# Kernel optimization log

Measured on AMD Instinct MI355X. Metric: run time of the kernel, lower is better.

## Reference

```python
import jax, jax.numpy as jnp
import numpy as np

N = 50000      # nodes
E = 400000     # edges
IN = 128       # in_channels
HID = 64       # hidden_channels (per head)
H = 4          # heads
OUT = 10       # classes
G = 64         # graphs in batch


def setup_inputs() -> dict:
    key = jax.random.key(0)
    ks = jax.random.split(key, 32)
    s = 0.05
    inp = {
        "x": jax.random.normal(ks[0], (N, IN), dtype=jnp.float32),
        "edge_index": jax.random.randint(ks[1], (2, E), 0, N, dtype=jnp.int32),
        "batch": jnp.sort(jax.random.randint(ks[2], (N,), 0, G, dtype=jnp.int32)),
    }
    # TransformerConv layer 1 params (in=IN -> heads*HID)
    d1 = H * HID
    inp["Wq1"] = jax.random.normal(ks[3], (IN, d1)) * s
    inp["bq1"] = jnp.zeros((d1,), jnp.float32)
    inp["Wk1"] = jax.random.normal(ks[4], (IN, d1)) * s
    inp["bk1"] = jnp.zeros((d1,), jnp.float32)
    inp["Wv1"] = jax.random.normal(ks[5], (IN, d1)) * s
    inp["bv1"] = jnp.zeros((d1,), jnp.float32)
    inp["Ws1"] = jax.random.normal(ks[6], (IN, d1)) * s   # root/skip weight
    inp["bs1"] = jnp.zeros((d1,), jnp.float32)
    # TransformerConv layer 2 params (in=H*HID -> heads*HID)
    inp["Wq2"] = jax.random.normal(ks[7], (d1, d1)) * s
    inp["bq2"] = jnp.zeros((d1,), jnp.float32)
    inp["Wk2"] = jax.random.normal(ks[8], (d1, d1)) * s
    inp["bk2"] = jnp.zeros((d1,), jnp.float32)
    inp["Wv2"] = jax.random.normal(ks[9], (d1, d1)) * s
    inp["bv2"] = jnp.zeros((d1,), jnp.float32)
    inp["Ws2"] = jax.random.normal(ks[10], (d1, d1)) * s
    inp["bs2"] = jnp.zeros((d1,), jnp.float32)
    # final classifier
    inp["Wl"] = jax.random.normal(ks[11], (d1, OUT)) * s
    inp["bl"] = jnp.zeros((OUT,), jnp.float32)
    return inp


def transformer_conv(x, src, dst, Wq, bq, Wk, bk, Wv, bv, Ws, bs):
    """PyG TransformerConv (concat=True, root_weight=True, beta=None, eval mode).
    src = edge_index[0] (source j), dst = edge_index[1] (target i).
    """
    n = x.shape[0]
    q = (x @ Wq + bq).reshape(n, H, HID)
    k = (x @ Wk + bk).reshape(n, H, HID)
    v = (x @ Wv + bv).reshape(n, H, HID)
    # per-edge attention logits [E, H]
    alpha = jnp.einsum('ehc,ehc->eh', q[dst], k[src]) / np.sqrt(HID).astype(np.float32)
    # scatter-softmax over incoming edges of each target node
    amax = jax.ops.segment_max(alpha, dst, num_segments=n)           # [N, H], -inf for isolated
    ex = jnp.exp(alpha - amax[dst])                                   # [E, H]
    denom = jax.ops.segment_sum(ex, dst, num_segments=n) + 1e-16      # [N, H]
    w = ex / denom[dst]                                               # normalized alpha [E, H]
    # scatter-sum aggregation of weighted values
    out = jax.ops.segment_sum(w[:, :, None] * v[src], dst, num_segments=n)  # [N, H, HID]
    out = out.reshape(n, H * HID)
    return out + (x @ Ws + bs)  # root/skip connection


def reference(x, edge_index, batch,
              Wq1, bq1, Wk1, bk1, Wv1, bv1, Ws1, bs1,
              Wq2, bq2, Wk2, bk2, Wv2, bv2, Ws2, bs2,
              Wl, bl):
    src, dst = edge_index[0], edge_index[1]
    h = jax.nn.elu(transformer_conv(x, src, dst, Wq1, bq1, Wk1, bk1, Wv1, bv1, Ws1, bs1))
    h = jax.nn.elu(transformer_conv(h, src, dst, Wq2, bq2, Wk2, bk2, Wv2, bv2, Ws2, bs2))
    # global mean pool per graph
    sums = jax.ops.segment_sum(h, batch, num_segments=G)              # [G, H*HID]
    cnt = jax.ops.segment_sum(jnp.ones((h.shape[0],), h.dtype), batch, num_segments=G)
    pooled = sums / jnp.maximum(cnt, 1.0)[:, None]
    logits = pooled @ Wl + bl
    return jax.nn.log_softmax(logits, axis=-1)
```

## Files before the change

kernel.cpp:

```cpp
#include <hip/hip_runtime.h>
#include <math.h>

constexpr int NN   = 50000;
constexpr int NE   = 400000;
constexpr int INC  = 128;
constexpr int NH   = 4;
constexpr int D1   = 256;
constexpr int D4   = 1024;
constexpr int NOUT = 10;
constexpr int NG   = 64;
constexpr int NB_SCAN = (NN + 255) / 256;


typedef __attribute__((ext_vector_type(8))) short bf16x8;
typedef __attribute__((ext_vector_type(4))) float f32x4;
typedef __attribute__((ext_vector_type(2))) float f32x2;

__device__ __forceinline__ short f2b(float f) {
  union { float f; unsigned int i; } v; v.f = f;
  unsigned int x = v.i;
  return (short)((x + 0x7FFFu + ((x >> 16) & 1u)) >> 16);
}
__device__ __forceinline__ float b2f(short u) {
  union { unsigned int i; float f; } v; v.i = ((unsigned int)(unsigned short)u) << 16;
  return v.f;
}
__device__ __forceinline__ float4 ld4b(const short* p) {
  short4 u = *(const short4*)p;
  return make_float4(b2f(u.x), b2f(u.y), b2f(u.z), b2f(u.w));
}
__device__ __forceinline__ int cvt_pk_bf16(float lo, float hi) {
  int r;
  asm volatile("v_cvt_pk_bf16_f32 %0, %1, %2" : "=v"(r) : "v"(lo), "v"(hi));
  return r;
}
__device__ __forceinline__ int pk_fp8x4(float a, float b, float c, float d) {
  int v = __builtin_amdgcn_cvt_pk_fp8_f32(a, b, 0, false);
  v = __builtin_amdgcn_cvt_pk_fp8_f32(c, d, v, true);
  return v;
}

__device__ __forceinline__ void gld_lds16(const short* g, short* l) {
  __builtin_amdgcn_global_load_lds(
      (const __attribute__((address_space(1))) unsigned int*)g,
      (__attribute__((address_space(3))) unsigned int*)l, 16, 0, 0);
}

constexpr int CVT_XB  = (NN * INC / 4 + 255) / 256;
constexpr int CVT_W1B = (4 * D1 * INC / 8 + 255) / 256;
constexpr int CVT_W2B = (4 * D1 * D1 / 8 + 255) / 256;
constexpr int CVT_BB  = 8;
constexpr int CVT_DB  = (NN + 255) / 256;
constexpr int CVT_FB  = 1;

__device__ __forceinline__ void wt_one8(const float* Wq, const float* Wk,
    const float* Wv, const float* Ws, short* Wt, int kbits, int i) {
  const int K = 1 << kbits;
  const int row = i >> (kbits - 3);
  const int k0 = (i & ((K >> 3) - 1)) << 3;
  int seg, n;
  if (row < 256)      { seg = 0; n = row; }
  else if (row < 768) { int j = row - 256, off = j & 7;
                        seg = (off >= 4) ? 2 : 1; n = (j >> 3) * 4 + (off & 3); }
  else                { seg = 3; n = row - 768; }
  const float* W = (seg == 0) ? Wq : (seg == 1) ? Wk : (seg == 2) ? Wv : Ws;
  short o[8];
#pragma unroll
  for (int kk = 0; kk < 8; kk++) o[kk] = f2b(W[(size_t)(k0 + kk) * D1 + n]);
  int4 pk;
  short* ps = (short*)&pk;
#pragma unroll
  for (int kk = 0; kk < 8; kk++) ps[kk] = o[kk];
  *(int4*)(Wt + (size_t)row * K + k0) = pk;
}

__global__ void cvt_all_k(const float* __restrict__ x, short* __restrict__ Xb,
    const float* __restrict__ Wq1, const float* __restrict__ Wk1,
    const float* __restrict__ Wv1, const float* __restrict__ Ws1,
    const float* __restrict__ Wq2, const float* __restrict__ Wk2,
    const float* __restrict__ Wv2, const float* __restrict__ Ws2,
    short* __restrict__ Wtc1, short* __restrict__ Wtc2,
    const float* __restrict__ bq1, const float* __restrict__ bk1,
    const float* __restrict__ bv1, const float* __restrict__ bs1,
    const float* __restrict__ bq2, const float* __restrict__ bk2,
    const float* __restrict__ bv2, const float* __restrict__ bs2,
    float* __restrict__ bc1, float* __restrict__ bc2,
    int* __restrict__ deg, unsigned int* __restrict__ desc) {
  const int b = blockIdx.x;
  const int t = threadIdx.x;
  if (b < CVT_XB) {
    int i = (b * 256 + t) * 4;
    if (i >= NN * INC) return;
    float4 v = *(const float4*)(x + i);
    short4 o; o.x = f2b(v.x); o.y = f2b(v.y); o.z = f2b(v.z); o.w = f2b(v.w);
    *(short4*)(Xb + i) = o;
  } else if (b < CVT_XB + CVT_W1B) {
    int i = (b - CVT_XB) * 256 + t;
    if (i < 4 * D1 * INC / 8) wt_one8(Wq1, Wk1, Wv1, Ws1, Wtc1, 7, i);
  } else if (b < CVT_XB + CVT_W1B + CVT_W2B) {
    int i = (b - CVT_XB - CVT_W1B) * 256 + t;
    if (i < 4 * D1 * D1 / 8) wt_one8(Wq2, Wk2, Wv2, Ws2, Wtc2, 8, i);
  } else if (b < CVT_XB + CVT_W1B + CVT_W2B + CVT_BB) {
    int i = (b - CVT_XB - CVT_W1B - CVT_W2B) * 256 + t;
    if (i >= 2 * D4) return;
    int row = i & (D4 - 1);
    const float* bq = (i < D4) ? bq1 : bq2;
    const float* bk = (i < D4) ? bk1 : bk2;
    const float* bv = (i < D4) ? bv1 : bv2;
    const float* bs = (i < D4) ? bs1 : bs2;
    float v;
    if (row < 256) v = bq[row];
    else if (row < 768) {
      int j = row - 256, grp = j >> 3, off = j & 7;
      int ch = grp * 4 + (off & 3);
      v = (off < 4) ? bk[ch] : bv[ch];
    } else v = bs[row - 768];
    ((i < D4) ? bc1 : bc2)[row] = v;
  } else if (b < CVT_XB + CVT_W1B + CVT_W2B + CVT_BB + CVT_DB) {
    int i = (b - CVT_XB - CVT_W1B - CVT_W2B - CVT_BB) * 256 + t;
    if (i < NN) deg[i] = 0;
  } else {
    if (t < NB_SCAN) desc[t] = 0u;
  }
}

__global__ void deg_count(const int* __restrict__ dst, int* __restrict__ deg) {
  int e = blockIdx.x * 256 + threadIdx.x;
  if (e < NE) atomicAdd(&deg[dst[e]], 1);
}

__global__ __launch_bounds__(256) void scan_k(const int* __restrict__ deg,
    const int* __restrict__ batch, unsigned int* __restrict__ desc,
    int* __restrict__ rowstart, int* __restrict__ cursor, int* __restrict__ gb) {
  const int b = blockIdx.x;
  const int t = threadIdx.x;
  if (b == NB_SCAN) {
    if (t > NG) return;
    int lo = 0, hi = NN;
    while (lo < hi) {
      int mid = (lo + hi) >> 1;
      if (batch[mid] < t) lo = mid + 1; else hi = mid;
    }
    gb[t] = lo;
    return;
  }
  __shared__ int sh[256];
  __shared__ int base_s;
  const int i = b * 256 + t;
  const int v = (i < NN) ? deg[i] : 0;
  sh[t] = v;
  __syncthreads();
  for (int off = 1; off < 256; off <<= 1) {
    int o = (t >= off) ? sh[t - off] : 0;
    __syncthreads();
    sh[t] += o;
    __syncthreads();
  }
  const int incl = sh[t];
  const int aggr = sh[255];
  if (t == 0) {
    if (b == 0) {
      __hip_atomic_store(&desc[0], ((unsigned int)aggr << 2) | 2u,
                         __ATOMIC_RELEASE, __HIP_MEMORY_SCOPE_AGENT);
      base_s = 0;
    } else {
      __hip_atomic_store(&desc[b], ((unsigned int)aggr << 2) | 1u,
                         __ATOMIC_RELEASE, __HIP_MEMORY_SCOPE_AGENT);
      int base = 0;
      int j = b - 1;
      while (j >= 0) {
        unsigned int d = __hip_atomic_load(&desc[j], __ATOMIC_ACQUIRE,
                                           __HIP_MEMORY_SCOPE_AGENT);
        unsigned int st = d & 3u;
        if (st == 2u)      { base += (int)(d >> 2); break; }
        else if (st == 1u) { base += (int)(d >> 2); j--; }
        else               { __builtin_amdgcn_s_sleep(2); }
      }
      __hip_atomic_store(&desc[b], ((unsigned int)(base + aggr) << 2) | 2u,
                         __ATOMIC_RELEASE, __HIP_MEMORY_SCOPE_AGENT);
      base_s = base;
    }
  }
  __syncthreads();
  const int excl = base_s + incl - v;
  if (i <= NN) rowstart[i] = excl;
  if (i < NN)  cursor[i]   = excl;
}

__global__ void scatter_k(const int* __restrict__ src, const int* __restrict__ dst,
    int* __restrict__ cursor, int* __restrict__ esrc) {
  int e = blockIdx.x * 256 + threadIdx.x;
  if (e >= NE) return;
  int d = dst[e];
  int pos = atomicAdd(&cursor[d], 1);
  esrc[pos] = src[e];
}

constexpr int CLDS = 136;

__global__ __launch_bounds__(256, 4) void gemm_mfma(
    const short* __restrict__ Xb, const short* __restrict__ Wt,
    const float* __restrict__ bias, short* __restrict__ QS,
    unsigned char* __restrict__ KV8, int M, int K) {
  __shared__ short smem[16384];
  const int bx = blockIdx.x;
  const int by = blockIdx.y;
  const int m_tile = (bx & 7) + (by << 3);
  const int n_tile = bx >> 3;
  const int m0 = m_tile * 128;
  if (m0 >= M) return;
  const int n0 = n_tile * 128;

  const int t    = threadIdx.x;
  const int lane = t & 63;
  const int wv   = t >> 6;
  const int wm   = (wv >> 1) * 64;
  const int wn   = (wv & 1) * 64;
  const int quad = lane >> 4;
  const int l16  = lane & 15;
  const int lrow = lane >> 2;
  const int lseg = lane & 3;

  const int swz_w = (lseg ^ ((lrow >> 1) & 3)) * 8;
  const int swz_r = (quad ^ ((l16 >> 1) & 3)) * 8;

  f32x4 acc[4][4] = {};

  {
#pragma unroll
    for (int j = 0; j < 2; ++j) {
      const int rb = (wv * 2 + j) * 16;
      int gm = m0 + rb + lrow;
      gm = gm < M ? gm : M - 1;
      gld_lds16(Xb + (size_t)gm * K + swz_w,              &smem[rb * 32]);
      gld_lds16(Wt + (size_t)(n0 + rb + lrow) * K + swz_w, &smem[4096 + rb * 32]);
    }
  }
  __syncthreads();

  int cur = 0;
  for (int k0 = 0; k0 < K; k0 += 32) {
    if (k0 + 32 < K) {
      short* An = &smem[(cur ^ 1) * 8192];
      short* Bn = &smem[(cur ^ 1) * 8192 + 4096];
#pragma unroll
      for (int j = 0; j < 2; ++j) {
        const int rb = (wv * 2 + j) * 16;
        int gm = m0 + rb + lrow;
        gm = gm < M ? gm : M - 1;
        gld_lds16(Xb + (size_t)gm * K + k0 + 32 + swz_w,              &An[rb * 32]);
        gld_lds16(Wt + (size_t)(n0 + rb + lrow) * K + k0 + 32 + swz_w, &Bn[rb * 32]);
      }
    }
    {
      const short* Ac = &smem[cur * 8192];
      const short* Bc = &smem[cur * 8192 + 4096];
      bf16x8 a[4], b[4];
#pragma unroll
      for (int mi = 0; mi < 4; mi++)
        a[mi] = *(const bf16x8*)(&Ac[(wm + mi * 16 + l16) * 32 + swz_r]);
#pragma unroll
      for (int nj = 0; nj < 4; nj++)
        b[nj] = *(const bf16x8*)(&Bc[(wn + nj * 16 + l16) * 32 + swz_r]);
#pragma unroll
      for (int mi = 0; mi < 4; mi++)
#pragma unroll
        for (int nj = 0; nj < 4; nj++)
          acc[mi][nj] = __builtin_amdgcn_mfma_f32_16x16x32_bf16(b[nj], a[mi], acc[mi][nj], 0, 0, 0);
    }
    __syncthreads();
    cur ^= 1;
  }

  const bool isKV = (n_tile >= 2) && (n_tile <= 5);
  float4 bz[4];
#pragma unroll
  for (int nj = 0; nj < 4; nj++)
    bz[nj] = *(const float4*)(bias + n0 + wn + nj * 16 + quad * 4);
  const int kv_base = n0 - 256;
  const int qs_base = (n_tile < 2) ? n0 : (n0 - 512);

#pragma unroll
  for (int p = 0; p < 2; ++p) {
    if ((wv >> 1) == p) {
      if (isKV) {
        unsigned char* cs = (unsigned char*)smem;
#pragma unroll
        for (int mi = 0; mi < 4; mi++) {
          const int row = mi * 16 + l16;
#pragma unroll
          for (int nj = 0; nj < 4; nj++) {
            const int colb = wn + nj * 16 + quad * 4;
            const int pk = pk_fp8x4(acc[mi][nj][0] + bz[nj].x, acc[mi][nj][1] + bz[nj].y,
                                    acc[mi][nj][2] + bz[nj].z, acc[mi][nj][3] + bz[nj].w);
            *(int*)(cs + row * 136 + colb) = pk;
          }
        }
      } else {
#pragma unroll
        for (int mi = 0; mi < 4; mi++) {
          const int row = mi * 16 + l16;
#pragma unroll
          for (int nj = 0; nj < 4; nj++) {
            const int col = wn + nj * 16 + quad * 4;
            int2 o;
            o.x = cvt_pk_bf16(acc[mi][nj][0] + bz[nj].x, acc[mi][nj][1] + bz[nj].y);
            o.y = cvt_pk_bf16(acc[mi][nj][2] + bz[nj].z, acc[mi][nj][3] + bz[nj].w);
            *(int2*)(&smem[row * CLDS + col]) = o;
          }
        }
      }
    }
    __syncthreads();
    if (isKV) {
      const unsigned char* cs = (const unsigned char*)smem;
#pragma unroll
      for (int it = 0; it < 4; ++it) {
        const int chunk = it * 256 + t;
        const int row = chunk >> 4;
        const int cb  = (chunk & 15) * 8;
        const int gm  = m0 + p * 64 + row;
        if (gm < M)
          *(int2*)(KV8 + (size_t)gm * 512 + kv_base + cb) = *(const int2*)(cs + row * 136 + cb);
      }
    } else {
#pragma unroll
      for (int it = 0; it < 4; ++it) {
        const int chunk = it * 256 + t;
        const int row = chunk >> 4;
        const int cc  = (chunk & 15) * 8;
        const int gm  = m0 + p * 64 + row;
        if (gm < M)
          *(int4*)(QS + (size_t)gm * 512 + qs_base + cc) = *(const int4*)(&smem[row * CLDS + cc]);
      }
    }
    if (p == 0) __syncthreads();
  }
}

__device__ __forceinline__ f32x2 cvt_lo(int x) { return __builtin_amdgcn_cvt_pk_f32_fp8(x, false); }
__device__ __forceinline__ f32x2 cvt_hi(int x) { return __builtin_amdgcn_cvt_pk_f32_fp8(x, true); }

template <int CTRL>
__device__ __forceinline__ float ror_add(float x) {
  int y = __builtin_amdgcn_update_dpp(0, __float_as_int(x), CTRL, 0xF, 0xF, true);
  return x + __int_as_float(y);
}
__device__ __forceinline__ float red16(float x) {
  x = ror_add<0x121>(x);
  x = ror_add<0x122>(x);
  x = ror_add<0x124>(x);
  x = ror_add<0x128>(x);
  return x;
}

#define SC2 (0.125f * 1.44269504088896341f)

__device__ __forceinline__ float edge_score(const int2 x, f32x2 q01, f32x2 q23,
                                            f32x2& vv01, f32x2& vv23) {
  f32x2 kk01 = cvt_lo(x.x), kk23 = cvt_hi(x.x);
  vv01 = cvt_lo(x.y); vv23 = cvt_hi(x.y);
  f32x2 dd = q01 * kk01;
  dd += q23 * kk23;
  return red16(dd.x + dd.y);
}

template <typename TOUT>
__device__ __forceinline__ void st1(TOUT* p, float v);
template <> __device__ __forceinline__ void st1<float>(float* p, float v) { *p = v; }
template <> __device__ __forceinline__ void st1<short>(short* p, float v) { *p = f2b(v); }

template <typename TOUT>
__global__ __launch_bounds__(256) void node_attn(
    const int* __restrict__ rowstart, const int* __restrict__ esrc,
    const short* __restrict__ QS, const unsigned char* __restrict__ KV8,
    TOUT* __restrict__ out) {
  const int nid = blockIdx.x * 4 + (threadIdx.x >> 6);
  if (nid >= NN) return;
  const int t  = threadIdx.x & 63;
  const int c0 = t * 4;
  const int r0 = __builtin_amdgcn_readfirstlane(rowstart[nid]);
  const int r1 = __builtin_amdgcn_readfirstlane(rowstart[nid + 1]);
  const short4 qu = *(const short4*)(QS + (size_t)nid * 512 + c0);
  const f32x2 q01 = {b2f(qu.x) * SC2, b2f(qu.y) * SC2};
  const f32x2 q23 = {b2f(qu.z) * SC2, b2f(qu.w) * SC2};
  const unsigned char* kvb = KV8 + t * 8;
  float m = -INFINITY, denom = 0.f;
  f32x2 a01 = {0.f, 0.f}, a23 = {0.f, 0.f};
  int r = r0;
  for (; r + 7 < r1; r += 8) {
    const int e0 = __builtin_amdgcn_readfirstlane(esrc[r + 0]);
    const int e1 = __builtin_amdgcn_readfirstlane(esrc[r + 1]);
    const int e2 = __builtin_amdgcn_readfirstlane(esrc[r + 2]);
    const int e3 = __builtin_amdgcn_readfirstlane(esrc[r + 3]);
    const int e4 = __builtin_amdgcn_readfirstlane(esrc[r + 4]);
    const int e5 = __builtin_amdgcn_readfirstlane(esrc[r + 5]);
    const int e6 = __builtin_amdgcn_readfirstlane(esrc[r + 6]);
    const int e7 = __builtin_amdgcn_readfirstlane(esrc[r + 7]);
    const int2 x0 = *(const int2*)(kvb + (size_t)e0 * 512);
    const int2 x1 = *(const int2*)(kvb + (size_t)e1 * 512);
    const int2 x2 = *(const int2*)(kvb + (size_t)e2 * 512);
    const int2 x3 = *(const int2*)(kvb + (size_t)e3 * 512);
    const int2 x4 = *(const int2*)(kvb + (size_t)e4 * 512);
    const int2 x5 = *(const int2*)(kvb + (size_t)e5 * 512);
    const int2 x6 = *(const int2*)(kvb + (size_t)e6 * 512);
    const int2 x7 = *(const int2*)(kvb + (size_t)e7 * 512);
    f32x2 v01_0, v23_0, v01_1, v23_1, v01_2, v23_2, v01_3, v23_3;
    f32x2 v01_4, v23_4, v01_5, v23_5, v01_6, v23_6, v01_7, v23_7;
    const float s0 = edge_score(x0, q01, q23, v01_0, v23_0);
    const float s1 = edge_score(x1, q01, q23, v01_1, v23_1);
    const float s2 = edge_score(x2, q01, q23, v01_2, v23_2);
    const float s3 = edge_score(x3, q01, q23, v01_3, v23_3);
    const float s4 = edge_score(x4, q01, q23, v01_4, v23_4);
    const float s5 = edge_score(x5, q01, q23, v01_5, v23_5);
    const float s6 = edge_score(x6, q01, q23, v01_6, v23_6);
    const float s7 = edge_score(x7, q01, q23, v01_7, v23_7);
    const float t01 = fmaxf(s0, s1), t23 = fmaxf(s2, s3);
    const float t45 = fmaxf(s4, s5), t67 = fmaxf(s6, s7);
    const float nm = fmaxf(fmaxf(m, fmaxf(t01, t23)), fmaxf(t45, t67));
    const float sc  = exp2f(m - nm);
    const float ex0 = exp2f(s0 - nm);
    const float ex1 = exp2f(s1 - nm);
    const float ex2 = exp2f(s2 - nm);
    const float ex3 = exp2f(s3 - nm);
    const float ex4 = exp2f(s4 - nm);
    const float ex5 = exp2f(s5 - nm);
    const float ex6 = exp2f(s6 - nm);
    const float ex7 = exp2f(s7 - nm);
    denom = denom * sc + ((ex0 + ex1) + (ex2 + ex3)) + ((ex4 + ex5) + (ex6 + ex7));
    const f32x2 scv = {sc, sc};
    a01 = a01 * scv; a23 = a23 * scv;
    a01 += f32x2{ex0, ex0} * v01_0; a23 += f32x2{ex0, ex0} * v23_0;
    a01 += f32x2{ex1, ex1} * v01_1; a23 += f32x2{ex1, ex1} * v23_1;
    a01 += f32x2{ex2, ex2} * v01_2; a23 += f32x2{ex2, ex2} * v23_2;
    a01 += f32x2{ex3, ex3} * v01_3; a23 += f32x2{ex3, ex3} * v23_3;
    a01 += f32x2{ex4, ex4} * v01_4; a23 += f32x2{ex4, ex4} * v23_4;
    a01 += f32x2{ex5, ex5} * v01_5; a23 += f32x2{ex5, ex5} * v23_5;
    a01 += f32x2{ex6, ex6} * v01_6; a23 += f32x2{ex6, ex6} * v23_6;
    a01 += f32x2{ex7, ex7} * v01_7; a23 += f32x2{ex7, ex7} * v23_7;
    m = nm;
  }
  for (; r + 3 < r1; r += 4) {
    const int e0 = __builtin_amdgcn_readfirstlane(esrc[r + 0]);
    const int e1 = __builtin_amdgcn_readfirstlane(esrc[r + 1]);
    const int e2 = __builtin_amdgcn_readfirstlane(esrc[r + 2]);
    const int e3 = __builtin_amdgcn_readfirstlane(esrc[r + 3]);
    const int2 x0 = *(const int2*)(kvb + (size_t)e0 * 512);
    const int2 x1 = *(const int2*)(kvb + (size_t)e1 * 512);
    const int2 x2 = *(const int2*)(kvb + (size_t)e2 * 512);
    const int2 x3 = *(const int2*)(kvb + (size_t)e3 * 512);
    f32x2 v01_0, v23_0, v01_1, v23_1, v01_2, v23_2, v01_3, v23_3;
    const float s0 = edge_score(x0, q01, q23, v01_0, v23_0);
    const float s1 = edge_score(x1, q01, q23, v01_1, v23_1);
    const float s2 = edge_score(x2, q01, q23, v01_2, v23_2);
    const float s3 = edge_score(x3, q01, q23, v01_3, v23_3);
    const float nm = fmaxf(fmaxf(m, fmaxf(s0, s1)), fmaxf(s2, s3));
    const float sc  = exp2f(m - nm);
    const float ex0 = exp2f(s0 - nm);
    const float ex1 = exp2f(s1 - nm);
    const float ex2 = exp2f(s2 - nm);
    const float ex3 = exp2f(s3 - nm);
    denom = denom * sc + ex0 + ex1 + ex2 + ex3;
    const f32x2 scv = {sc, sc};
    a01 = a01 * scv; a23 = a23 * scv;
    a01 += f32x2{ex0, ex0} * v01_0; a23 += f32x2{ex0, ex0} * v23_0;
    a01 += f32x2{ex1, ex1} * v01_1; a23 += f32x2{ex1, ex1} * v23_1;
    a01 += f32x2{ex2, ex2} * v01_2; a23 += f32x2{ex2, ex2} * v23_2;
    a01 += f32x2{ex3, ex3} * v01_3; a23 += f32x2{ex3, ex3} * v23_3;
    m = nm;
  }
  for (; r < r1; r++) {
    const int e0 = __builtin_amdgcn_readfirstlane(esrc[r]);
    const int2 x0 = *(const int2*)(kvb + (size_t)e0 * 512);
    f32x2 v01_0, v23_0;
    const float s0 = edge_score(x0, q01, q23, v01_0, v23_0);
    const float nm = fmaxf(m, s0);
    const float sc  = exp2f(m - nm);
    const float ex0 = exp2f(s0 - nm);
    denom = denom * sc + ex0;
    const f32x2 scv = {sc, sc};
    a01 = a01 * scv; a23 = a23 * scv;
    a01 += f32x2{ex0, ex0} * v01_0; a23 += f32x2{ex0, ex0} * v23_0;
    m = nm;
  }
  const float inv = 1.0f / (denom + 1e-16f);
  const float4 sk = ld4b(QS + (size_t)nid * 512 + 256 + c0);
  float o0 = a01.x * inv + sk.x;
  float o1 = a01.y * inv + sk.y;
  float o2 = a23.x * inv + sk.z;
  float o3 = a23.y * inv + sk.w;
  o0 = o0 > 0.f ? o0 : expm1f(o0);
  o1 = o1 > 0.f ? o1 : expm1f(o1);
  o2 = o2 > 0.f ? o2 : expm1f(o2);
  o3 = o3 > 0.f ? o3 : expm1f(o3);
  TOUT* p = out + (size_t)nid * D1 + c0;
  st1<TOUT>(p + 0, o0); st1<TOUT>(p + 1, o1);
  st1<TOUT>(p + 2, o2); st1<TOUT>(p + 3, o3);
}

__global__ __launch_bounds__(1024) void pool_head_k(const short* __restrict__ h,
    const int* __restrict__ gb, const float* __restrict__ Wl,
    const float* __restrict__ bl, float* __restrict__ out) {
  __shared__ float sh4[1024];
  __shared__ float mlds[D1];
  __shared__ float lgs[NOUT];
  const int g = blockIdx.x;
  const int t = threadIdx.x;
  const int c = t & (D1 - 1);
  const int no = t >> 8;
  const int a = gb[g], b = gb[g + 1];
  float s = 0.f;
  for (int n = a + no; n < b; n += 4) s += b2f(h[(size_t)n * D1 + c]);
  sh4[t] = s;
  __syncthreads();
  if (no == 0) {
    const float inv = 1.0f / fmaxf((float)(b - a), 1.0f);
    mlds[c] = (sh4[c] + sh4[c + 256] + sh4[c + 512] + sh4[c + 768]) * inv;
  }
  __syncthreads();
  if (t < 64) {
#pragma unroll
    for (int o = 0; o < NOUT; o++) {
      float p = 0.f;
#pragma unroll
      for (int q = 0; q < 4; q++)
        p += mlds[t + q * 64] * Wl[(t + q * 64) * NOUT + o];
#pragma unroll
      for (int off = 1; off < 64; off <<= 1) p += __shfl_xor(p, off, 64);
      if (t == 0) lgs[o] = p + bl[o];
    }
    if (t == 0) {
      float mx = -INFINITY;
#pragma unroll
      for (int o = 0; o < NOUT; o++) mx = fmaxf(mx, lgs[o]);
      float se = 0.f;
#pragma unroll
      for (int o = 0; o < NOUT; o++) se += __expf(lgs[o] - mx);
      const float lse = mx + logf(se);
#pragma unroll
      for (int o = 0; o < NOUT; o++) out[g * NOUT + o] = lgs[o] - lse;
    }
  }
}

extern "C" void kernel_launch(void* const* d_in, const int* in_sizes, int n_in,
                              void* d_out, int out_size, void* d_ws, size_t ws_size,
                              hipStream_t stream) {
  const float* x   = (const float*)d_in[0];
  const int* ei    = (const int*)d_in[1];
  const int* batch = (const int*)d_in[2];
  const float* Wq1 = (const float*)d_in[3];  const float* bq1 = (const float*)d_in[4];
  const float* Wk1 = (const float*)d_in[5];  const float* bk1 = (const float*)d_in[6];
  const float* Wv1 = (const float*)d_in[7];  const float* bv1 = (const float*)d_in[8];
  const float* Ws1 = (const float*)d_in[9];  const float* bs1 = (const float*)d_in[10];
  const float* Wq2 = (const float*)d_in[11]; const float* bq2 = (const float*)d_in[12];
  const float* Wk2 = (const float*)d_in[13]; const float* bk2 = (const float*)d_in[14];
  const float* Wv2 = (const float*)d_in[15]; const float* bv2 = (const float*)d_in[16];
  const float* Ws2 = (const float*)d_in[17]; const float* bs2 = (const float*)d_in[18];
  const float* Wl  = (const float*)d_in[19]; const float* bl  = (const float*)d_in[20];

  const int* srcIdx = ei;
  const int* dstIdx = ei + NE;

  float* ws = (float*)d_ws;
  const size_t SZ_NODE = (size_t)NN * D1;
  short* H2b  = (short*)ws;
  float* bc1  = ws + SZ_NODE;
  float* bc2  = bc1 + D4;
  short* Xb   = (short*)(bc2 + D4);
  short* H1b  = Xb + (size_t)NN * INC;
  short* QS   = H1b + SZ_NODE;
  short* Wtc1 = QS + (size_t)NN * 512;
  short* Wtc2 = Wtc1 + (size_t)D4 * INC;
  unsigned char* KV8 = (unsigned char*)(Wtc2 + (size_t)D4 * D1);
  int* ip      = (int*)(KV8 + (size_t)NN * 512);
  int* deg     = ip;
  unsigned int* desc = (unsigned int*)(deg + NN);
  int* rowstart= (int*)(desc + 256);
  int* cursor  = rowstart + NN + 1;
  int* esrc    = cursor + NN;
  int* gb      = esrc + NE;

  const int mtiles = (NN + 127) / 128;
  const dim3 gemmGrid(64, (mtiles + 7) / 8);
  const int edgeBlocks = (NE + 255) / 256;
  const int aggBlocks  = (NN + 3) / 4;
  const int cvtBlocks  = CVT_XB + CVT_W1B + CVT_W2B + CVT_BB + CVT_DB + CVT_FB;

  cvt_all_k<<<cvtBlocks, 256, 0, stream>>>(x, Xb,
      Wq1, Wk1, Wv1, Ws1, Wq2, Wk2, Wv2, Ws2, Wtc1, Wtc2,
      bq1, bk1, bv1, bs1, bq2, bk2, bv2, bs2, bc1, bc2, deg, desc);

  deg_count<<<edgeBlocks, 256, 0, stream>>>(dstIdx, deg);
  scan_k<<<NB_SCAN + 1, 256, 0, stream>>>(deg, batch, desc, rowstart, cursor, gb);
  scatter_k<<<edgeBlocks, 256, 0, stream>>>(srcIdx, dstIdx, cursor, esrc);

  gemm_mfma<<<gemmGrid, 256, 0, stream>>>(Xb, Wtc1, bc1, QS, KV8, NN, INC);
  node_attn<short><<<aggBlocks, 256, 0, stream>>>(rowstart, esrc, QS, KV8, H1b);

  gemm_mfma<<<gemmGrid, 256, 0, stream>>>(H1b, Wtc2, bc2, QS, KV8, NN, D1);
  node_attn<short><<<aggBlocks, 256, 0, stream>>>(rowstart, esrc, QS, KV8, H2b);

  pool_head_k<<<NG, 1024, 0, stream>>>(H2b, gb, Wl, bl, (float*)d_out);
}
```

Before: 397.8 us.

## Parallelize global mean pool across node chunks and use warp-wide scan lookback

The pool+head kernel, which used one block per graph (64 blocks), is split into a pool kernel with one block per 64-node chunk that atomically accumulates per-graph sums, plus a single-block head kernel for the classifier and log-softmax. The sums buffer is zeroed in the conversion kernel. Separately, the decoupled-lookback scan now has a full wavefront examine 64 predecessor descriptors at once using ballots and shuffles, where a single thread previously walked them one by one. The aim is more parallelism in pooling and shorter serial lookback chains, at the cost of an extra launch and float atomics that make the pooled sums order-dependent.

New measurement: 336.2 us. -15.5%, faster.

```diff
diff --git a/kernel.cpp b/kernel.cpp
--- a/kernel.cpp
+++ b/kernel.cpp
@@ -52,6 +52,7 @@
 constexpr int CVT_BB  = 8;
 constexpr int CVT_DB  = (NN + 255) / 256;
 constexpr int CVT_FB  = 1;
+constexpr int CVT_SB  = (NG * D1 + 255) / 256;
 
 __device__ __forceinline__ void wt_one8(const float* Wq, const float* Wk,
     const float* Wv, const float* Ws, short* Wt, int kbits, int i) {
@@ -85,7 +86,8 @@
     const float* __restrict__ bq2, const float* __restrict__ bk2,
     const float* __restrict__ bv2, const float* __restrict__ bs2,
     float* __restrict__ bc1, float* __restrict__ bc2,
-    int* __restrict__ deg, unsigned int* __restrict__ desc) {
+    int* __restrict__ deg, unsigned int* __restrict__ desc,
+    float* __restrict__ sums) {
   const int b = blockIdx.x;
   const int t = threadIdx.x;
   if (b < CVT_XB) {
@@ -119,8 +121,11 @@
   } else if (b < CVT_XB + CVT_W1B + CVT_W2B + CVT_BB + CVT_DB) {
     int i = (b - CVT_XB - CVT_W1B - CVT_W2B - CVT_BB) * 256 + t;
     if (i < NN) deg[i] = 0;
+  } else if (b < CVT_XB + CVT_W1B + CVT_W2B + CVT_BB + CVT_DB + CVT_FB) {
+    if (t < NB_SCAN) desc[t] = 0u;
   } else {
-    if (t < NB_SCAN) desc[t] = 0u;
+    int i = (b - CVT_XB - CVT_W1B - CVT_W2B - CVT_BB - CVT_DB - CVT_FB) * 256 + t;
+    if (i < NG * D1) sums[i] = 0.f;
   }
 }
 
@@ -158,24 +163,42 @@
   }
   const int incl = sh[t];
   const int aggr = sh[255];
-  if (t == 0) {
-    if (b == 0) {
-      __hip_atomic_store(&desc[0], ((unsigned int)aggr << 2) | 2u,
-                         __ATOMIC_RELEASE, __HIP_MEMORY_SCOPE_AGENT);
-      base_s = 0;
-    } else {
-      __hip_atomic_store(&desc[b], ((unsigned int)aggr << 2) | 1u,
-                         __ATOMIC_RELEASE, __HIP_MEMORY_SCOPE_AGENT);
-      int base = 0;
-      int j = b - 1;
-      while (j >= 0) {
-        unsigned int d = __hip_atomic_load(&desc[j], __ATOMIC_ACQUIRE,
-                                           __HIP_MEMORY_SCOPE_AGENT);
-        unsigned int st = d & 3u;
-        if (st == 2u)      { base += (int)(d >> 2); break; }
-        else if (st == 1u) { base += (int)(d >> 2); j--; }
-        else               { __builtin_amdgcn_s_sleep(2); }
+  if (t == 0)
+    __hip_atomic_store(&desc[b], ((unsigned int)aggr << 2) | (b == 0 ? 2u : 1u),
+                       __ATOMIC_RELEASE, __HIP_MEMORY_SCOPE_AGENT);
+  if (b == 0) {
+    if (t == 0) base_s = 0;
+  } else if (t < 64) {
+    int base = 0;
+    int j = b - 1;
+    for (;;) {
+      const int idx = j - t;
+      const unsigned int d = (idx >= 0)
+          ? __hip_atomic_load(&desc[idx], __ATOMIC_ACQUIRE,
+                              __HIP_MEMORY_SCOPE_AGENT)
+          : 2u;
+      const unsigned int st = d & 3u;
+      const unsigned long long m_incl = __ballot(st == 2u);
+      const unsigned long long m_inv  = __ballot(st == 0u);
+      const int fi = m_incl ? (__ffsll((unsigned long long)m_incl) - 1) : 64;
+      const int fv = m_inv  ? (__ffsll((unsigned long long)m_inv ) - 1) : 64;
+      if (fi < fv) {
+        int contrib = (t <= fi) ? (int)(d >> 2) : 0;
+#pragma unroll
+        for (int off = 1; off < 64; off <<= 1) contrib += __shfl_xor(contrib, off, 64);
+        base += contrib;
+        break;
+      } else if (fv == 64) {
+        int contrib = (int)(d >> 2);
+#pragma unroll
+        for (int off = 1; off < 64; off <<= 1) contrib += __shfl_xor(contrib, off, 64);
+        base += contrib;
+        j -= 64;
+      } else {
+        __builtin_amdgcn_s_sleep(1);
       }
+    }
+    if (t == 0) {
       __hip_atomic_store(&desc[b], ((unsigned int)(base + aggr) << 2) | 2u,
                          __ATOMIC_RELEASE, __HIP_MEMORY_SCOPE_AGENT);
       base_s = base;
@@ -498,48 +521,54 @@
   st1<TOUT>(p + 2, o2); st1<TOUT>(p + 3, o3);
 }
 
-__global__ __launch_bounds__(1024) void pool_head_k(const short* __restrict__ h,
+__global__ __launch_bounds__(256) void pool_k(const short* __restrict__ h,
+    const int* __restrict__ batch, const int* __restrict__ gb,
+    float* __restrict__ sums) {
+  const int c = threadIdx.x;
+  const int n0 = blockIdx.x * 64;
+  const int n1 = min(n0 + 64, NN);
+  const int g0 = batch[n0];
+  const int g1 = batch[n1 - 1];
+  for (int g = g0; g <= g1; ++g) {
+    const int a = max(gb[g], n0);
+    const int b = min(gb[g + 1], n1);
+    if (b <= a) continue;
+    float s0 = 0.f, s1 = 0.f, s2 = 0.f, s3 = 0.f;
+    int n = a;
+    for (; n + 3 < b; n += 4) {
+      s0 += b2f(h[(size_t)(n + 0) * D1 + c]);
+      s1 += b2f(h[(size_t)(n + 1) * D1 + c]);
+      s2 += b2f(h[(size_t)(n + 2) * D1 + c]);
+      s3 += b2f(h[(size_t)(n + 3) * D1 + c]);
+    }
+    for (; n < b; ++n) s0 += b2f(h[(size_t)n * D1 + c]);
+    atomicAdd(&sums[(size_t)g * D1 + c], (s0 + s1) + (s2 + s3));
+  }
+}
+
+__global__ __launch_bounds__(640) void head_k(const float* __restrict__ sums,
     const int* __restrict__ gb, const float* __restrict__ Wl,
     const float* __restrict__ bl, float* __restrict__ out) {
-  __shared__ float sh4[1024];
-  __shared__ float mlds[D1];
-  __shared__ float lgs[NOUT];
-  const int g = blockIdx.x;
+  __shared__ float logits[NG][NOUT];
   const int t = threadIdx.x;
-  const int c = t & (D1 - 1);
-  const int no = t >> 8;
-  const int a = gb[g], b = gb[g + 1];
-  float s = 0.f;
-  for (int n = a + no; n < b; n += 4) s += b2f(h[(size_t)n * D1 + c]);
-  sh4[t] = s;
+  if (t < NG * NOUT) {
+    int g = t / NOUT, o = t % NOUT;
+    float inv = 1.0f / fmaxf((float)(gb[g + 1] - gb[g]), 1.0f);
+    float acc = 0.f;
+    for (int k = 0; k < D1; k++) acc += sums[(size_t)g * D1 + k] * Wl[k * NOUT + o];
+    logits[g][o] = acc * inv + bl[o];
+  }
   __syncthreads();
-  if (no == 0) {
-    const float inv = 1.0f / fmaxf((float)(b - a), 1.0f);
-    mlds[c] = (sh4[c] + sh4[c + 256] + sh4[c + 512] + sh4[c + 768]) * inv;
-  }
-  __syncthreads();
-  if (t < 64) {
-#pragma unroll
-    for (int o = 0; o < NOUT; o++) {
-      float p = 0.f;
-#pragma unroll
-      for (int q = 0; q < 4; q++)
-        p += mlds[t + q * 64] * Wl[(t + q * 64) * NOUT + o];
-#pragma unroll
-      for (int off = 1; off < 64; off <<= 1) p += __shfl_xor(p, off, 64);
-      if (t == 0) lgs[o] = p + bl[o];
-    }
-    if (t == 0) {
-      float mx = -INFINITY;
-#pragma unroll
-      for (int o = 0; o < NOUT; o++) mx = fmaxf(mx, lgs[o]);
-      float se = 0.f;
-#pragma unroll
-      for (int o = 0; o < NOUT; o++) se += __expf(lgs[o] - mx);
-      const float lse = mx + logf(se);
-#pragma unroll
-      for (int o = 0; o < NOUT; o++) out[g * NOUT + o] = lgs[o] - lse;
-    }
+  if (t < NG) {
+    float mx = -INFINITY;
+#pragma unroll
+    for (int o = 0; o < NOUT; o++) mx = fmaxf(mx, logits[t][o]);
+    float s = 0.f;
+#pragma unroll
+    for (int o = 0; o < NOUT; o++) s += __expf(logits[t][o] - mx);
+    float lse = mx + logf(s);
+#pragma unroll
+    for (int o = 0; o < NOUT; o++) out[t * NOUT + o] = logits[t][o] - lse;
   }
 }
 
@@ -565,7 +594,8 @@
   float* ws = (float*)d_ws;
   const size_t SZ_NODE = (size_t)NN * D1;
   short* H2b  = (short*)ws;
-  float* bc1  = ws + SZ_NODE;
+  float* sums = ws + SZ_NODE;
+  float* bc1  = sums + (size_t)NG * D1;
   float* bc2  = bc1 + D4;
   short* Xb   = (short*)(bc2 + D4);
   short* H1b  = Xb + (size_t)NN * INC;
@@ -585,11 +615,11 @@
   const dim3 gemmGrid(64, (mtiles + 7) / 8);
   const int edgeBlocks = (NE + 255) / 256;
   const int aggBlocks  = (NN + 3) / 4;
-  const int cvtBlocks  = CVT_XB + CVT_W1B + CVT_W2B + CVT_BB + CVT_DB + CVT_FB;
+  const int cvtBlocks  = CVT_XB + CVT_W1B + CVT_W2B + CVT_BB + CVT_DB + CVT_FB + CVT_SB;
 
   cvt_all_k<<<cvtBlocks, 256, 0, stream>>>(x, Xb,
       Wq1, Wk1, Wv1, Ws1, Wq2, Wk2, Wv2, Ws2, Wtc1, Wtc2,
-      bq1, bk1, bv1, bs1, bq2, bk2, bv2, bs2, bc1, bc2, deg, desc);
+      bq1, bk1, bv1, bs1, bq2, bk2, bv2, bs2, bc1, bc2, deg, desc, sums);
 
   deg_count<<<edgeBlocks, 256, 0, stream>>>(dstIdx, deg);
   scan_k<<<NB_SCAN + 1, 256, 0, stream>>>(deg, batch, desc, rowstart, cursor, gb);
@@ -601,5 +631,6 @@
   gemm_mfma<<<gemmGrid, 256, 0, stream>>>(H1b, Wtc2, bc2, QS, KV8, NN, D1);
   node_attn<short><<<aggBlocks, 256, 0, stream>>>(rowstart, esrc, QS, KV8, H2b);
 
-  pool_head_k<<<NG, 1024, 0, stream>>>(H2b, gb, Wl, bl, (float*)d_out);
-}
+  pool_k<<<(NN + 63) / 64, 256, 0, stream>>>(H2b, batch, gb, sums);
+  head_k<<<1, 640, 0, stream>>>(sums, gb, Wl, bl, (float*)d_out);
+}
```
